# Kernel tuning notes

Hardware: AMD Instinct MI355X
Metric: run time of the kernel (lower is better)

## Reference

```python
import jax, jax.numpy as jnp
import numpy as np

D_MODEL = 1024
N_HEADS = 16
HEAD_DIM = D_MODEL // N_HEADS


def setup_inputs() -> dict:
    key = jax.random.key(0)
    ks = jax.random.split(key, 5)
    x = jax.random.normal(ks[0], (4, 2048, D_MODEL), dtype=jnp.float32)
    s = 1.0 / np.sqrt(D_MODEL)
    W_qkv = jax.random.normal(ks[1], (D_MODEL, 3 * D_MODEL), dtype=jnp.float32) * s
    b_qkv = jnp.zeros((3 * D_MODEL,), dtype=jnp.float32)
    W_proj = jax.random.normal(ks[2], (D_MODEL, D_MODEL), dtype=jnp.float32) * s
    b_proj = jnp.zeros((D_MODEL,), dtype=jnp.float32)
    return {"x": x, "W_qkv": W_qkv, "b_qkv": b_qkv, "W_proj": W_proj, "b_proj": b_proj}


def reference(x, W_qkv, b_qkv, W_proj, b_proj):
    B, T, C = x.shape
    H, Dh = N_HEADS, HEAD_DIM
    qkv = x @ W_qkv + b_qkv                      # [B,T,3C]
    q, k, v = jnp.split(qkv, 3, axis=-1)
    # [B,T,C] -> [B,H,T,Dh]
    q = q.reshape(B, T, H, Dh).transpose(0, 2, 1, 3)
    k = k.reshape(B, T, H, Dh).transpose(0, 2, 1, 3)
    v = v.reshape(B, T, H, Dh).transpose(0, 2, 1, 3)
    scale = 1.0 / np.sqrt(Dh)
    att = jnp.einsum("bhqd,bhkd->bhqk", q, k) * scale
    causal = jnp.tril(jnp.ones((T, T), dtype=bool))
    att = jnp.where(causal, att, -jnp.inf)
    att = jax.nn.softmax(att, axis=-1)
    y = jnp.einsum("bhqk,bhkd->bhqd", att, v)    # [B,H,T,Dh]
    y = y.transpose(0, 2, 1, 3).reshape(B, T, C)
    return y @ W_proj + b_proj
```

## Files before the change

### kernel.cpp

```cpp
#include <hip/hip_runtime.h>
#include <hip/hip_bf16.h>
#include <cstdint>
#include <math.h>

#define DM   1024
#define NH   16
#define DH   64
#define BB   4
#define TT   2048
#define MTOT (BB*TT)

using short8 = __attribute__((ext_vector_type(8))) short;
using f32x4  = __attribute__((ext_vector_type(4))) float;

__device__ __forceinline__ f32x4 mfma16(short8 a, short8 b, f32x4 c) {
  return __builtin_amdgcn_mfma_f32_16x16x32_bf16(a, b, c, 0, 0, 0);
}

typedef const __attribute__((address_space(1))) unsigned int* as1_u32p;
typedef __attribute__((address_space(3))) unsigned int*       as3_u32p;

__device__ __forceinline__ void gl_lds16(const void* g, void* l) {
  __builtin_amdgcn_global_load_lds(
      (as1_u32p)(reinterpret_cast<uintptr_t>(g)),
      (as3_u32p)((unsigned int)(reinterpret_cast<uintptr_t>(l))),
      16, 0, 0);
}

__device__ __forceinline__ int swz64(int row, int col) {
  return row*64 + ((((col >> 3) ^ (row & 7)) << 3) | (col & 7));
}

__device__ __forceinline__ unsigned pkbf(float a, float b) {
  __hip_bfloat162 h = __float22bfloat162_rn(make_float2(a, b));
  return *reinterpret_cast<unsigned*>(&h);
}

__device__ __forceinline__ unsigned xor16v(unsigned x, bool odd) {
  unsigned a = x, b = x;
  asm("v_permlane16_swap_b32 %0, %1" : "+v"(a), "+v"(b));
  return odd ? a : b;
}
__device__ __forceinline__ unsigned swap32sel(unsigned d, unsigned s, bool odd) {
  asm("v_permlane32_swap_b32 %0, %1" : "+v"(d), "+v"(s));
  return odd ? s : d;
}

__device__ __forceinline__ short8 ldsr_o0(unsigned a) {
  short8 r; asm volatile("ds_read_b128 %0, %1" : "=v"(r) : "v"(a)); return r;
}
__device__ __forceinline__ short8 ldsr_o1(unsigned a) {
  short8 r; asm volatile("ds_read_b128 %0, %1 offset:2048" : "=v"(r) : "v"(a)); return r;
}
__device__ __forceinline__ short8 ldsr_o2(unsigned a) {
  short8 r; asm volatile("ds_read_b128 %0, %1 offset:4096" : "=v"(r) : "v"(a)); return r;
}
__device__ __forceinline__ short8 ldsr_o3(unsigned a) {
  short8 r; asm volatile("ds_read_b128 %0, %1 offset:6144" : "=v"(r) : "v"(a)); return r;
}

#define LGKM0  do { asm volatile("s_waitcnt lgkmcnt(0)"); __builtin_amdgcn_sched_barrier(0); } while(0)
#define VMCNT6 do { __builtin_amdgcn_sched_barrier(0); asm volatile("s_waitcnt vmcnt(6)"); __builtin_amdgcn_sched_barrier(0); } while(0)
#define VMCNT0 do { __builtin_amdgcn_sched_barrier(0); asm volatile("s_waitcnt vmcnt(0)"); __builtin_amdgcn_sched_barrier(0); } while(0)
#define BARRIER do { __builtin_amdgcn_s_barrier(); __builtin_amdgcn_sched_barrier(0); } while(0)

__global__ __launch_bounds__(256) void k_cvt(const float* __restrict__ in,
                                             __hip_bfloat16* __restrict__ out, int n8) {
  int i = blockIdx.x * 256 + threadIdx.x;
  if (i >= n8) return;
  const float* p = in + (size_t)i * 8;
  short8 o;
#pragma unroll
  for (int j = 0; j < 8; ++j) {
    __hip_bfloat16 h = __float2bfloat16(p[j]);
    o[j] = *reinterpret_cast<short*>(&h);
  }
  *reinterpret_cast<short8*>(out + (size_t)i * 8) = o;
}

__global__ __launch_bounds__(256) void k_transpose_cvt(const float* __restrict__ W,
                                                       __hip_bfloat16* __restrict__ Wt,
                                                       int K, int N) {
  __shared__ float tbuf[32][33];
  const int n0 = blockIdx.x * 32, k0 = blockIdx.y * 32;
  const int tx = threadIdx.x & 31, ty = threadIdx.x >> 5;
#pragma unroll
  for (int i = 0; i < 4; ++i)
    tbuf[ty + i*8][tx] = W[(size_t)(k0 + ty + i*8) * N + n0 + tx];
  __syncthreads();
#pragma unroll
  for (int i = 0; i < 4; ++i)
    Wt[(size_t)(n0 + ty + i*8) * K + k0 + tx] = __float2bfloat16(tbuf[tx][ty + i*8]);
}

__global__ __launch_bounds__(512, 2) void k_gemm2(const __hip_bfloat16* __restrict__ A,
                                                  const __hip_bfloat16* __restrict__ Bt,
                                                  const float* __restrict__ bias,
                                                  __hip_bfloat16* __restrict__ Qb,
                                                  __hip_bfloat16* __restrict__ Kb,
                                                  __hip_bfloat16* __restrict__ Vtb) {
  __shared__ __hip_bfloat16 As[3][256 * 64];
  __shared__ __hip_bfloat16 Bs[3][128 * 64];
  const int tid = threadIdx.x;
  const int l = tid & 63, w = tid >> 6;
  const int lr = l & 15, lg = l >> 4;
  const int wm = w >> 1, wn = w & 1;
  const int m0 = blockIdx.x * 256, n0 = blockIdx.y * 128;

  const int srow = tid >> 3;
  const int scol = (((tid & 7) ^ (srow & 7)) << 3);
  const size_t aoffs = (size_t)(m0 + srow) * 1024 + scol;
  const size_t boffs = (size_t)(n0 + srow) * 1024 + scol;
  const int ldst = tid * 8;

  auto stage = [&](int t, int s) {
    const int k0 = t * 64;
    __hip_bfloat16* as_ = &As[s][0];
    __hip_bfloat16* bs_ = &Bs[s][0];
#pragma unroll
    for (int rd = 0; rd < 4; ++rd)
      gl_lds16(A + aoffs + (size_t)rd * 65536 + k0, as_ + rd * 4096 + ldst);
#pragma unroll
    for (int rd = 0; rd < 2; ++rd)
      gl_lds16(Bt + boffs + (size_t)rd * 65536 + k0, bs_ + rd * 4096 + ldst);
  };

  const unsigned asLds = (unsigned)(uintptr_t)&As[0][0];
  const unsigned bsLds = (unsigned)(uintptr_t)&Bs[0][0];
  const unsigned aBase = asLds + 2u * ((wm*64 + lr) * 64 + ((lg ^ (lr & 7)) << 3));
  const unsigned bBase = bsLds + 2u * ((wn*64 + lr) * 64 + ((lg ^ (lr & 7)) << 3));

  stage(0, 0);
  stage(1, 1);
  VMCNT6;
  BARRIER;

  f32x4 acc[4][4] = {};
  short8 a_[4][2], b_[2][2];

#pragma unroll
  for (int t = 0; t < 16; ++t) {
    const int s = t % 3;
    const unsigned aB0 = aBase + (unsigned)s * 32768u;
    const unsigned aB1 = aB0 ^ 64u;
    const unsigned bB0 = bBase + (unsigned)s * 16384u;
    const unsigned bB1 = bB0 ^ 64u;
    if (t + 2 < 16) stage(t + 2, (t + 2) % 3);
    a_[0][0] = ldsr_o0(aB0); a_[1][0] = ldsr_o1(aB0); a_[2][0] = ldsr_o2(aB0); a_[3][0] = ldsr_o3(aB0);
    a_[0][1] = ldsr_o0(aB1); a_[1][1] = ldsr_o1(aB1); a_[2][1] = ldsr_o2(aB1); a_[3][1] = ldsr_o3(aB1);
    b_[0][0] = ldsr_o0(bB0); b_[1][0] = ldsr_o1(bB0);
    b_[0][1] = ldsr_o0(bB1); b_[1][1] = ldsr_o1(bB1);
    LGKM0;
    __builtin_amdgcn_s_setprio(1);
#pragma unroll
    for (int m = 0; m < 4; ++m)
#pragma unroll
      for (int n = 0; n < 2; ++n)
#pragma unroll
        for (int ks = 0; ks < 2; ++ks)
          acc[m][n] = mfma16(a_[m][ks], b_[n][ks], acc[m][n]);
    __builtin_amdgcn_s_setprio(0);
    b_[0][0] = ldsr_o2(bB0); b_[1][0] = ldsr_o3(bB0);
    b_[0][1] = ldsr_o2(bB1); b_[1][1] = ldsr_o3(bB1);
    LGKM0;
    __builtin_amdgcn_s_setprio(1);
#pragma unroll
    for (int m = 0; m < 4; ++m)
#pragma unroll
      for (int n = 0; n < 2; ++n)
#pragma unroll
        for (int ks = 0; ks < 2; ++ks)
          acc[m][n + 2] = mfma16(a_[m][ks], b_[n][ks], acc[m][n + 2]);
    __builtin_amdgcn_s_setprio(0);
    if (t <= 13) { VMCNT6; }
    else if (t == 14) { VMCNT0; }
    BARRIER;
  }

  __syncthreads();
  __hip_bfloat16* reg = &As[0][0] + w * 4096;
  const int colbase = n0 + wn * 64;
  const int which = colbase >> 10;
  const int hh = (colbase >> 6) & 15;
  const float qs = 0.18033688011112042f;
#pragma unroll
  for (int n = 0; n < 4; ++n) {
    const int lc = n * 16 + lr;
    const float bv = bias[colbase + lc];
#pragma unroll
    for (int m = 0; m < 4; ++m) {
#pragma unroll
      for (int r = 0; r < 4; ++r) {
        const int lrow = m * 16 + lg * 4 + r;
        float v = acc[m][n][r] + bv;
        if (which == 0) v *= qs;
        const __hip_bfloat16 hv = __float2bfloat16(v);
        if (which == 2) reg[swz64(lc, lrow)] = hv;
        else            reg[swz64(lrow, lc)] = hv;
      }
    }
  }
  const int rowbase = m0 + wm * 64;
  const int b = rowbase >> 11;
  const size_t bh = (size_t)b * 16 + hh;
  const int g = l >> 2, i = l & 3;
  if (which < 2) {
    __hip_bfloat16* base = (which == 0) ? Qb : Kb;
#pragma unroll
    for (int j = 0; j < 4; ++j) {
      const int lrow = j * 16 + g;
      const int t = (rowbase & 2047) + lrow;
      __hip_bfloat16* dst = base + (bh * TT + t) * 64 + i * 16;
      short8 y0 = *reinterpret_cast<const short8*>(&reg[swz64(lrow, i * 16)]);
      short8 y1 = *reinterpret_cast<const short8*>(&reg[swz64(lrow, i * 16 + 8)]);
      *reinterpret_cast<short8*>(dst) = y0;
      *reinterpret_cast<short8*>(dst + 8) = y1;
    }
  } else {
#pragma unroll
    for (int j = 0; j < 4; ++j) {
      const int dd = j * 16 + g;
      const int t = (rowbase & 2047) + i * 16;
      __hip_bfloat16* dst = Vtb + (bh * 64 + dd) * TT + t;
      short8 y0 = *reinterpret_cast<const short8*>(&reg[swz64(dd, i * 16)]);
      short8 y1 = *reinterpret_cast<const short8*>(&reg[swz64(dd, i * 16 + 8)]);
      *reinterpret_cast<short8*>(dst) = y0;
      *reinterpret_cast<short8*>(dst + 8) = y1;
    }
  }
}

__global__ __launch_bounds__(256) void k_gemm(const __hip_bfloat16* __restrict__ A,
                                              const __hip_bfloat16* __restrict__ Bt,
                                              const float* __restrict__ bias,
                                              float* __restrict__ outF) {
  __shared__ __hip_bfloat16 As[128 * 64];
  __shared__ __hip_bfloat16 Bs[128 * 64];
  const int tid = threadIdx.x;
  const int l = tid & 63, w = tid >> 6;
  const int lr = l & 15, lg = l >> 4;
  const int wr = w >> 1, wc = w & 1;
  const int m0 = blockIdx.x * 128, n0 = blockIdx.y * 128;
  f32x4 acc[4][4] = {};
  for (int k0 = 0; k0 < 1024; k0 += 64) {
#pragma unroll
    for (int it = 0; it < 4; ++it) {
      int e = it * 2048 + tid * 8;
      int row = e >> 6;
      int lcol = ((((e >> 3) & 7) ^ (row & 7)) << 3);
      gl_lds16(A + (size_t)(m0 + row) * 1024 + k0 + lcol, &As[e]);
    }
#pragma unroll
    for (int it = 0; it < 4; ++it) {
      int e = it * 2048 + tid * 8;
      int row = e >> 6;
      int lcol = ((((e >> 3) & 7) ^ (row & 7)) << 3);
      gl_lds16(Bt + (size_t)(n0 + row) * 1024 + k0 + lcol, &Bs[e]);
    }
    __syncthreads();
#pragma unroll
    for (int ks = 0; ks < 2; ++ks) {
      short8 af[4], bf[4];
#pragma unroll
      for (int m = 0; m < 4; ++m)
        af[m] = *reinterpret_cast<const short8*>(&As[swz64(wr*64 + m*16 + lr, ks*32 + lg*8)]);
#pragma unroll
      for (int n = 0; n < 4; ++n)
        bf[n] = *reinterpret_cast<const short8*>(&Bs[swz64(wc*64 + n*16 + lr, ks*32 + lg*8)]);
#pragma unroll
      for (int m = 0; m < 4; ++m)
#pragma unroll
        for (int n = 0; n < 4; ++n)
          acc[m][n] = mfma16(af[m], bf[n], acc[m][n]);
    }
    __syncthreads();
  }
#pragma unroll
  for (int n = 0; n < 4; ++n) {
    const int col = n0 + wc*64 + n*16 + lr;
    const float bv = bias[col];
#pragma unroll
    for (int m = 0; m < 4; ++m)
#pragma unroll
      for (int r = 0; r < 4; ++r) {
        const int row = m0 + wr*64 + m*16 + lg*4 + r;
        outF[(size_t)row * 1024 + col] = acc[m][n][r] + bv;
      }
  }
}

__device__ __forceinline__ void tile_step(f32x4 s0, f32x4 s1, int kbase, int kmaxw, int qm,
                                          bool odd, short8 v0, short8 v1, short8 v2, short8 v3,
                                          f32x4 (&acc)[4], float& lrun) {
  if (kbase + 31 > kmaxw - 15) {
#pragma unroll
    for (int r = 0; r < 4; ++r) {
      if (kbase + r > qm)      s0[r] = -INFINITY;
      if (kbase + 16 + r > qm) s1[r] = -INFINITY;
    }
  }
  float p0 = __builtin_amdgcn_exp2f(s0[0]), p1 = __builtin_amdgcn_exp2f(s0[1]);
  float p2 = __builtin_amdgcn_exp2f(s0[2]), p3 = __builtin_amdgcn_exp2f(s0[3]);
  float p4 = __builtin_amdgcn_exp2f(s1[0]), p5 = __builtin_amdgcn_exp2f(s1[1]);
  float p6 = __builtin_amdgcn_exp2f(s1[2]), p7 = __builtin_amdgcn_exp2f(s1[3]);
  lrun += ((p0 + p1) + (p2 + p3)) + ((p4 + p5) + (p6 + p7));
  const unsigned u0 = pkbf(p0, p1);
  const unsigned u1 = pkbf(p2, p3);
  const unsigned u2 = pkbf(p4, p5);
  const unsigned u3 = pkbf(p6, p7);
  const unsigned e0 = xor16v(u0, odd);
  const unsigned e1 = xor16v(u1, odd);
  const unsigned e2 = xor16v(u2, odd);
  const unsigned e3 = xor16v(u3, odd);
  const unsigned ql0 = odd ? e0 : u0;
  const unsigned ql1 = odd ? e1 : u1;
  const unsigned ql2 = odd ? u0 : e0;
  const unsigned ql3 = odd ? u1 : e1;
  const unsigned qh0 = odd ? e2 : u2;
  const unsigned qh1 = odd ? e3 : u3;
  const unsigned qh2 = odd ? u2 : e2;
  const unsigned qh3 = odd ? u3 : e3;
  union { unsigned u[4]; short8 s; } pw;
  pw.u[0] = swap32sel(ql0, qh0, odd);
  pw.u[1] = swap32sel(ql1, qh1, odd);
  pw.u[2] = swap32sel(ql2, qh2, odd);
  pw.u[3] = swap32sel(ql3, qh3, odd);
  const short8 pf = pw.s;
  acc[0] = mfma16(v0, pf, acc[0]);
  acc[1] = mfma16(v1, pf, acc[1]);
  acc[2] = mfma16(v2, pf, acc[2]);
  acc[3] = mfma16(v3, pf, acc[3]);
}

__device__ __forceinline__ void store_tile(__hip_bfloat16* Ylds, f32x4 (&acc)[4],
                                           float lrun, int q0, int w, int l,
                                           int lr, int lg, int bh,
                                           __hip_bfloat16* __restrict__ Y) {
  lrun += __shfl_xor(lrun, 16);
  lrun += __shfl_xor(lrun, 32);
  const float inv = 1.f / lrun;
#pragma unroll
  for (int nb = 0; nb < 4; ++nb) {
#pragma unroll
    for (int r = 0; r < 4; ++r) {
      const int d = nb * 16 + lg * 4 + r;
      Ylds[swz64(lr, d)] = __float2bfloat16(acc[nb][r] * inv);
    }
  }
  const int rr = l >> 2, part = l & 3;
  const int trow = q0 + w * 16 + rr;
  const int b = bh >> 4, h = bh & 15;
  short8 y0 = *reinterpret_cast<const short8*>(&Ylds[swz64(rr, part * 16)]);
  short8 y1 = *reinterpret_cast<const short8*>(&Ylds[swz64(rr, part * 16 + 8)]);
  __hip_bfloat16* dst = Y + ((size_t)b * TT + trow) * 1024 + h * 64 + part * 16;
  *reinterpret_cast<short8*>(dst) = y0;
  *reinterpret_cast<short8*>(dst + 8) = y1;
}

__global__ __launch_bounds__(256, 4) void k_flash(const __hip_bfloat16* __restrict__ Qb,
                                                  const __hip_bfloat16* __restrict__ Kb,
                                                  const __hip_bfloat16* __restrict__ Vtb,
                                                  __hip_bfloat16* __restrict__ Y) {
  __shared__ __hip_bfloat16 Klds[128 * 64];
  __shared__ __hip_bfloat16 Vtlds[64 * 128];
  const int tid = threadIdx.x;
  const int l = tid & 63, w = tid >> 6;
  const int lr = l & 15, lg = l >> 4;
  const bool odd = (lg & 1);
  const int p  = blockIdx.x >> 6;
  const int bh = blockIdx.x & 63;
  const int q0A = p * 64, q0B = (31 - p) * 64;
  const __hip_bfloat16* Qp = Qb + (size_t)bh * TT * 64;
  const __hip_bfloat16* Kp = Kb + (size_t)bh * TT * 64;
  const __hip_bfloat16* Vp = Vtb + (size_t)bh * 64 * TT;
  const int qrowA = q0A + w * 16 + lr;
  const int qrowB = q0B + w * 16 + lr;
  const short8 qfA0 = *reinterpret_cast<const short8*>(Qp + (size_t)qrowA * 64 + lg * 8);
  const short8 qfA1 = *reinterpret_cast<const short8*>(Qp + (size_t)qrowA * 64 + 32 + lg * 8);
  const short8 qfB0 = *reinterpret_cast<const short8*>(Qp + (size_t)qrowB * 64 + lg * 8);
  const short8 qfB1 = *reinterpret_cast<const short8*>(Qp + (size_t)qrowB * 64 + 32 + lg * 8);
  f32x4 accA[4] = {}, accB[4] = {};
  float lA = 0.f, lB = 0.f;

  const int ka  = lr * 64 + ((lg ^ (lr & 7)) << 3);
  const int va  = lr * 128 + ((lg ^ (lr & 15)) << 3);

  const __hip_bfloat16* gk[4];
  const __hip_bfloat16* gv[4];
  __hip_bfloat16* lk[4];
  __hip_bfloat16* lv[4];
#pragma unroll
  for (int it = 0; it < 4; ++it) {
    int e = it * 2048 + tid * 8;
    int rowk = e >> 6;
    int lcolk = ((((e >> 3) & 7) ^ (rowk & 7)) << 3);
    gk[it] = Kp + (size_t)rowk * 64 + lcolk;
    lk[it] = &Klds[e];
    int rowv = e >> 7;
    int lcolv = ((((e >> 3) & 15) ^ (rowv & 15)) << 3);
    gv[it] = Vp + (size_t)rowv * TT + lcolv;
    lv[it] = &Vtlds[e];
  }

  const int kmaxwA = q0A + w * 16 + 15;
  const int kmaxwB = q0B + w * 16 + 15;
  const int qmA = qrowA - lg * 4;
  const int qmB = qrowB - lg * 4;
  const int nblk = (q0B + 63) / 128 + 1;
  for (int blk = 0; blk < nblk; ++blk) {
    const int kv0 = blk * 128;
#pragma unroll
    for (int it = 0; it < 4; ++it) {
      gl_lds16(gk[it], lk[it]);
      gk[it] += 128 * 64;
    }
#pragma unroll
    for (int it = 0; it < 4; ++it) {
      gl_lds16(gv[it], lv[it]);
      gv[it] += 128;
    }
    __syncthreads();
#pragma unroll
    for (int kci = 0; kci < 4; ++kci) {
      const int kbase = kv0 + kci * 32;
      if (kbase > kmaxwB) break;
      const int kb = ka + kci * 2048;
      const short8 kf00 = *reinterpret_cast<const short8*>(&Klds[kb]);
      const short8 kf10 = *reinterpret_cast<const short8*>(&Klds[kb + 1024]);
      const short8 kf01 = *reinterpret_cast<const short8*>(&Klds[kb ^ 32]);
      const short8 kf11 = *reinterpret_cast<const short8*>(&Klds[(kb + 1024) ^ 32]);
      f32x4 sB0 = {}, sB1 = {};
      sB0 = mfma16(kf00, qfB0, sB0);
      sB1 = mfma16(kf10, qfB0, sB1);
      sB0 = mfma16(kf01, qfB1, sB0);
      sB1 = mfma16(kf11, qfB1, sB1);
      const bool aAct = (kbase <= kmaxwA);
      f32x4 sA0 = {}, sA1 = {};
      if (aAct) {
        sA0 = mfma16(kf00, qfA0, sA0);
        sA1 = mfma16(kf10, qfA0, sA1);
        sA0 = mfma16(kf01, qfA1, sA0);
        sA1 = mfma16(kf11, qfA1, sA1);
      }
      const int vb = va ^ (kci * 32);
      const short8 v0 = *reinterpret_cast<const short8*>(&Vtlds[vb]);
      const short8 v1 = *reinterpret_cast<const short8*>(&Vtlds[vb + 2048]);
      const short8 v2 = *reinterpret_cast<const short8*>(&Vtlds[vb + 4096]);
      const short8 v3 = *reinterpret_cast<const short8*>(&Vtlds[vb + 6144]);
      tile_step(sB0, sB1, kbase, kmaxwB, qmB, odd, v0, v1, v2, v3, accB, lB);
      if (aAct)
        tile_step(sA0, sA1, kbase, kmaxwA, qmA, odd, v0, v1, v2, v3, accA, lA);
    }
    __syncthreads();
  }
  __hip_bfloat16* Ylds = Klds + w * 1024;
  store_tile(Ylds, accA, lA, q0A, w, l, lr, lg, bh, Y);
  store_tile(Ylds, accB, lB, q0B, w, l, lr, lg, bh, Y);
}

extern "C" void kernel_launch(void* const* d_in, const int* in_sizes, int n_in,
                              void* d_out, int out_size, void* d_ws, size_t ws_size,
                              hipStream_t stream) {
  const float* x     = (const float*)d_in[0];
  const float* Wqkv  = (const float*)d_in[1];
  const float* bqkv  = (const float*)d_in[2];
  const float* Wproj = (const float*)d_in[3];
  const float* bproj = (const float*)d_in[4];

  char* ws = (char*)d_ws;
  size_t off = 0;
  auto alloc = [&](size_t bytes) {
    char* p = ws + off;
    off += (bytes + 255) & ~(size_t)255;
    return p;
  };
  __hip_bfloat16* xb    = (__hip_bfloat16*)alloc((size_t)MTOT * 1024 * 2);
  __hip_bfloat16* wqkvT = (__hip_bfloat16*)alloc((size_t)3072 * 1024 * 2);
  __hip_bfloat16* wpT   = (__hip_bfloat16*)alloc((size_t)1024 * 1024 * 2);
  __hip_bfloat16* Qb    = (__hip_bfloat16*)alloc((size_t)64 * TT * 64 * 2);
  __hip_bfloat16* Kb    = (__hip_bfloat16*)alloc((size_t)64 * TT * 64 * 2);
  __hip_bfloat16* Vtb   = (__hip_bfloat16*)alloc((size_t)64 * TT * 64 * 2);
  __hip_bfloat16* Yb    = (__hip_bfloat16*)alloc((size_t)MTOT * 1024 * 2);

  k_cvt<<<(MTOT * 1024 / 8 + 255) / 256, 256, 0, stream>>>(x, xb, MTOT * 1024 / 8);
  k_transpose_cvt<<<dim3(3072 / 32, 1024 / 32), 256, 0, stream>>>(Wqkv, wqkvT, 1024, 3072);
  k_transpose_cvt<<<dim3(1024 / 32, 1024 / 32), 256, 0, stream>>>(Wproj, wpT, 1024, 1024);
  k_gemm2<<<dim3(32, 24), 512, 0, stream>>>(xb, wqkvT, bqkv, Qb, Kb, Vtb);
  k_flash<<<16 * 64, 256, 0, stream>>>(Qb, Kb, Vtb, Yb);
  k_gemm<<<dim3(64, 8), 256, 0, stream>>>(Yb, wpT, bproj, (float*)d_out);
}
```

Measured before the change: 166.3 us.

## Reuse pipelined 256x128 GEMM for output projection and simplify P-fragment permutes

New measurement: 152.3 us. 8.4% less time.

```diff
diff --git a/kernel.cpp b/kernel.cpp
--- a/kernel.cpp
+++ b/kernel.cpp
@@ -36,14 +36,11 @@
   return *reinterpret_cast<unsigned*>(&h);
 }
 
-__device__ __forceinline__ unsigned xor16v(unsigned x, bool odd) {
-  unsigned a = x, b = x;
+__device__ __forceinline__ void perm16p(unsigned &a, unsigned &b) {
   asm("v_permlane16_swap_b32 %0, %1" : "+v"(a), "+v"(b));
-  return odd ? a : b;
-}
-__device__ __forceinline__ unsigned swap32sel(unsigned d, unsigned s, bool odd) {
-  asm("v_permlane32_swap_b32 %0, %1" : "+v"(d), "+v"(s));
-  return odd ? s : d;
+}
+__device__ __forceinline__ void perm32p(unsigned &a, unsigned &b) {
+  asm("v_permlane32_swap_b32 %0, %1" : "+v"(a), "+v"(b));
 }
 
 __device__ __forceinline__ short8 ldsr_o0(unsigned a) {
@@ -93,9 +90,11 @@
     Wt[(size_t)(n0 + ty + i*8) * K + k0 + tx] = __float2bfloat16(tbuf[tx][ty + i*8]);
 }
 
+template <int EPI>
 __global__ __launch_bounds__(512, 2) void k_gemm2(const __hip_bfloat16* __restrict__ A,
                                                   const __hip_bfloat16* __restrict__ Bt,
                                                   const float* __restrict__ bias,
+                                                  float* __restrict__ outF,
                                                   __hip_bfloat16* __restrict__ Qb,
                                                   __hip_bfloat16* __restrict__ Kb,
                                                   __hip_bfloat16* __restrict__ Vtb) {
@@ -178,125 +177,82 @@
   }
 
   __syncthreads();
-  __hip_bfloat16* reg = &As[0][0] + w * 4096;
-  const int colbase = n0 + wn * 64;
-  const int which = colbase >> 10;
-  const int hh = (colbase >> 6) & 15;
-  const float qs = 0.18033688011112042f;
-#pragma unroll
-  for (int n = 0; n < 4; ++n) {
-    const int lc = n * 16 + lr;
-    const float bv = bias[colbase + lc];
-#pragma unroll
-    for (int m = 0; m < 4; ++m) {
-#pragma unroll
-      for (int r = 0; r < 4; ++r) {
-        const int lrow = m * 16 + lg * 4 + r;
-        float v = acc[m][n][r] + bv;
-        if (which == 0) v *= qs;
-        const __hip_bfloat16 hv = __float2bfloat16(v);
-        if (which == 2) reg[swz64(lc, lrow)] = hv;
-        else            reg[swz64(lrow, lc)] = hv;
+  if (EPI == 0) {
+    __hip_bfloat16* reg = &As[0][0] + w * 4096;
+    const int colbase = n0 + wn * 64;
+    const int which = colbase >> 10;
+    const int hh = (colbase >> 6) & 15;
+    const float qs = 0.18033688011112042f;
+#pragma unroll
+    for (int n = 0; n < 4; ++n) {
+      const int lc = n * 16 + lr;
+      const float bv = bias[colbase + lc];
+#pragma unroll
+      for (int m = 0; m < 4; ++m) {
+#pragma unroll
+        for (int r = 0; r < 4; ++r) {
+          const int lrow = m * 16 + lg * 4 + r;
+          float v = acc[m][n][r] + bv;
+          if (which == 0) v *= qs;
+          const __hip_bfloat16 hv = __float2bfloat16(v);
+          if (which == 2) reg[swz64(lc, lrow)] = hv;
+          else            reg[swz64(lrow, lc)] = hv;
+        }
       }
     }
-  }
-  const int rowbase = m0 + wm * 64;
-  const int b = rowbase >> 11;
-  const size_t bh = (size_t)b * 16 + hh;
-  const int g = l >> 2, i = l & 3;
-  if (which < 2) {
-    __hip_bfloat16* base = (which == 0) ? Qb : Kb;
-#pragma unroll
-    for (int j = 0; j < 4; ++j) {
-      const int lrow = j * 16 + g;
-      const int t = (rowbase & 2047) + lrow;
-      __hip_bfloat16* dst = base + (bh * TT + t) * 64 + i * 16;
-      short8 y0 = *reinterpret_cast<const short8*>(&reg[swz64(lrow, i * 16)]);
-      short8 y1 = *reinterpret_cast<const short8*>(&reg[swz64(lrow, i * 16 + 8)]);
-      *reinterpret_cast<short8*>(dst) = y0;
-      *reinterpret_cast<short8*>(dst + 8) = y1;
+    const int rowbase = m0 + wm * 64;
+    const int b = rowbase >> 11;
+    const size_t bh = (size_t)b * 16 + hh;
+    const int g = l >> 2, i = l & 3;
+    if (which < 2) {
+      __hip_bfloat16* base = (which == 0) ? Qb : Kb;
+#pragma unroll
+      for (int j = 0; j < 4; ++j) {
+        const int lrow = j * 16 + g;
+        const int t = (rowbase & 2047) + lrow;
+        __hip_bfloat16* dst = base + (bh * TT + t) * 64 + i * 16;
+        short8 y0 = *reinterpret_cast<const short8*>(&reg[swz64(lrow, i * 16)]);
+        short8 y1 = *reinterpret_cast<const short8*>(&reg[swz64(lrow, i * 16 + 8)]);
+        *reinterpret_cast<short8*>(dst) = y0;
+        *reinterpret_cast<short8*>(dst + 8) = y1;
+      }
+    } else {
+#pragma unroll
+      for (int j = 0; j < 4; ++j) {
+        const int dd = j * 16 + g;
+        const int t = (rowbase & 2047) + i * 16;
+        __hip_bfloat16* dst = Vtb + (bh * 64 + dd) * TT + t;
+        short8 y0 = *reinterpret_cast<const short8*>(&reg[swz64(dd, i * 16)]);
+        short8 y1 = *reinterpret_cast<const short8*>(&reg[swz64(dd, i * 16 + 8)]);
+        *reinterpret_cast<short8*>(dst) = y0;
+        *reinterpret_cast<short8*>(dst + 8) = y1;
+      }
     }
   } else {
 #pragma unroll
-    for (int j = 0; j < 4; ++j) {
-      const int dd = j * 16 + g;
-      const int t = (rowbase & 2047) + i * 16;
-      __hip_bfloat16* dst = Vtb + (bh * 64 + dd) * TT + t;
-      short8 y0 = *reinterpret_cast<const short8*>(&reg[swz64(dd, i * 16)]);
-      short8 y1 = *reinterpret_cast<const short8*>(&reg[swz64(dd, i * 16 + 8)]);
-      *reinterpret_cast<short8*>(dst) = y0;
-      *reinterpret_cast<short8*>(dst + 8) = y1;
-    }
-  }
-}
-
-__global__ __launch_bounds__(256) void k_gemm(const __hip_bfloat16* __restrict__ A,
-                                              const __hip_bfloat16* __restrict__ Bt,
-                                              const float* __restrict__ bias,
-                                              float* __restrict__ outF) {
-  __shared__ __hip_bfloat16 As[128 * 64];
-  __shared__ __hip_bfloat16 Bs[128 * 64];
-  const int tid = threadIdx.x;
-  const int l = tid & 63, w = tid >> 6;
-  const int lr = l & 15, lg = l >> 4;
-  const int wr = w >> 1, wc = w & 1;
-  const int m0 = blockIdx.x * 128, n0 = blockIdx.y * 128;
-  f32x4 acc[4][4] = {};
-  for (int k0 = 0; k0 < 1024; k0 += 64) {
-#pragma unroll
-    for (int it = 0; it < 4; ++it) {
-      int e = it * 2048 + tid * 8;
-      int row = e >> 6;
-      int lcol = ((((e >> 3) & 7) ^ (row & 7)) << 3);
-      gl_lds16(A + (size_t)(m0 + row) * 1024 + k0 + lcol, &As[e]);
-    }
-#pragma unroll
-    for (int it = 0; it < 4; ++it) {
-      int e = it * 2048 + tid * 8;
-      int row = e >> 6;
-      int lcol = ((((e >> 3) & 7) ^ (row & 7)) << 3);
-      gl_lds16(Bt + (size_t)(n0 + row) * 1024 + k0 + lcol, &Bs[e]);
-    }
-    __syncthreads();
-#pragma unroll
-    for (int ks = 0; ks < 2; ++ks) {
-      short8 af[4], bf[4];
+    for (int n = 0; n < 4; ++n) {
+      const int col = n0 + wn * 64 + n * 16 + lr;
+      const float bv = bias[col];
 #pragma unroll
       for (int m = 0; m < 4; ++m)
-        af[m] = *reinterpret_cast<const short8*>(&As[swz64(wr*64 + m*16 + lr, ks*32 + lg*8)]);
-#pragma unroll
-      for (int n = 0; n < 4; ++n)
-        bf[n] = *reinterpret_cast<const short8*>(&Bs[swz64(wc*64 + n*16 + lr, ks*32 + lg*8)]);
-#pragma unroll
-      for (int m = 0; m < 4; ++m)
-#pragma unroll
-        for (int n = 0; n < 4; ++n)
-          acc[m][n] = mfma16(af[m], bf[n], acc[m][n]);
-    }
-    __syncthreads();
-  }
-#pragma unroll
-  for (int n = 0; n < 4; ++n) {
-    const int col = n0 + wc*64 + n*16 + lr;
-    const float bv = bias[col];
-#pragma unroll
-    for (int m = 0; m < 4; ++m)
-#pragma unroll
-      for (int r = 0; r < 4; ++r) {
-        const int row = m0 + wr*64 + m*16 + lg*4 + r;
-        outF[(size_t)row * 1024 + col] = acc[m][n][r] + bv;
-      }
-  }
-}
-
-__device__ __forceinline__ void tile_step(f32x4 s0, f32x4 s1, int kbase, int kmaxw, int qm,
-                                          bool odd, short8 v0, short8 v1, short8 v2, short8 v3,
+#pragma unroll
+        for (int r = 0; r < 4; ++r) {
+          const int row = m0 + wm * 64 + m * 16 + lg * 4 + r;
+          outF[(size_t)row * 1024 + col] = acc[m][n][r] + bv;
+        }
+    }
+  }
+}
+
+__device__ __forceinline__ void tile_step(f32x4 s0, f32x4 s1, int kbase, int kmaxw, int qmb,
+                                          short8 v0, short8 v1, short8 v2, short8 v3,
                                           f32x4 (&acc)[4], float& lrun) {
   if (kbase + 31 > kmaxw - 15) {
 #pragma unroll
     for (int r = 0; r < 4; ++r) {
-      if (kbase + r > qm)      s0[r] = -INFINITY;
-      if (kbase + 16 + r > qm) s1[r] = -INFINITY;
+      const int off = (r & 1) + ((r & 2) << 2);
+      if (kbase + off > qmb)      s0[r] = -INFINITY;
+      if (kbase + 16 + off > qmb) s1[r] = -INFINITY;
     }
   }
   float p0 = __builtin_amdgcn_exp2f(s0[0]), p1 = __builtin_amdgcn_exp2f(s0[1]);
@@ -304,27 +260,16 @@
   float p4 = __builtin_amdgcn_exp2f(s1[0]), p5 = __builtin_amdgcn_exp2f(s1[1]);
   float p6 = __builtin_amdgcn_exp2f(s1[2]), p7 = __builtin_amdgcn_exp2f(s1[3]);
   lrun += ((p0 + p1) + (p2 + p3)) + ((p4 + p5) + (p6 + p7));
-  const unsigned u0 = pkbf(p0, p1);
-  const unsigned u1 = pkbf(p2, p3);
-  const unsigned u2 = pkbf(p4, p5);
-  const unsigned u3 = pkbf(p6, p7);
-  const unsigned e0 = xor16v(u0, odd);
-  const unsigned e1 = xor16v(u1, odd);
-  const unsigned e2 = xor16v(u2, odd);
-  const unsigned e3 = xor16v(u3, odd);
-  const unsigned ql0 = odd ? e0 : u0;
-  const unsigned ql1 = odd ? e1 : u1;
-  const unsigned ql2 = odd ? u0 : e0;
-  const unsigned ql3 = odd ? u1 : e1;
-  const unsigned qh0 = odd ? e2 : u2;
-  const unsigned qh1 = odd ? e3 : u3;
-  const unsigned qh2 = odd ? u2 : e2;
-  const unsigned qh3 = odd ? u3 : e3;
+  unsigned u0 = pkbf(p0, p1);
+  unsigned u1 = pkbf(p2, p3);
+  unsigned u2 = pkbf(p4, p5);
+  unsigned u3 = pkbf(p6, p7);
+  perm16p(u0, u1);
+  perm16p(u2, u3);
+  perm32p(u0, u2);
+  perm32p(u1, u3);
   union { unsigned u[4]; short8 s; } pw;
-  pw.u[0] = swap32sel(ql0, qh0, odd);
-  pw.u[1] = swap32sel(ql1, qh1, odd);
-  pw.u[2] = swap32sel(ql2, qh2, odd);
-  pw.u[3] = swap32sel(ql3, qh3, odd);
+  pw.u[0] = u0; pw.u[1] = u2; pw.u[2] = u1; pw.u[3] = u3;
   const short8 pf = pw.s;
   acc[0] = mfma16(v0, pf, acc[0]);
   acc[1] = mfma16(v1, pf, acc[1]);
@@ -366,7 +311,6 @@
   const int tid = threadIdx.x;
   const int l = tid & 63, w = tid >> 6;
   const int lr = l & 15, lg = l >> 4;
-  const bool odd = (lg & 1);
   const int p  = blockIdx.x >> 6;
   const int bh = blockIdx.x & 63;
   const int q0A = p * 64, q0B = (31 - p) * 64;
@@ -394,7 +338,10 @@
     int e = it * 2048 + tid * 8;
     int rowk = e >> 6;
     int lcolk = ((((e >> 3) & 7) ^ (rowk & 7)) << 3);
-    gk[it] = Kp + (size_t)rowk * 64 + lcolk;
+    int rk = rowk & 15;
+    int srk = (((rk >> 1) ^ (rk >> 3)) & 1) ? (rk ^ 10) : rk;
+    int rowks = (rowk & ~15) | srk;
+    gk[it] = Kp + (size_t)rowks * 64 + lcolk;
     lk[it] = &Klds[e];
     int rowv = e >> 7;
     int lcolv = ((((e >> 3) & 15) ^ (rowv & 15)) << 3);
@@ -404,8 +351,9 @@
 
   const int kmaxwA = q0A + w * 16 + 15;
   const int kmaxwB = q0B + w * 16 + 15;
-  const int qmA = qrowA - lg * 4;
-  const int qmB = qrowB - lg * 4;
+  const int base_lg = ((lg & 1) << 2) | (lg & 2);
+  const int qmbA = qrowA - base_lg;
+  const int qmbB = qrowB - base_lg;
   const int nblk = (q0B + 63) / 128 + 1;
   for (int blk = 0; blk < nblk; ++blk) {
     const int kv0 = blk * 128;
@@ -447,9 +395,9 @@
       const short8 v1 = *reinterpret_cast<const short8*>(&Vtlds[vb + 2048]);
       const short8 v2 = *reinterpret_cast<const short8*>(&Vtlds[vb + 4096]);
       const short8 v3 = *reinterpret_cast<const short8*>(&Vtlds[vb + 6144]);
-      tile_step(sB0, sB1, kbase, kmaxwB, qmB, odd, v0, v1, v2, v3, accB, lB);
+      tile_step(sB0, sB1, kbase, kmaxwB, qmbB, v0, v1, v2, v3, accB, lB);
       if (aAct)
-        tile_step(sA0, sA1, kbase, kmaxwA, qmA, odd, v0, v1, v2, v3, accA, lA);
+        tile_step(sA0, sA1, kbase, kmaxwA, qmbA, v0, v1, v2, v3, accA, lA);
     }
     __syncthreads();
   }
@@ -485,7 +433,8 @@
   k_cvt<<<(MTOT * 1024 / 8 + 255) / 256, 256, 0, stream>>>(x, xb, MTOT * 1024 / 8);
   k_transpose_cvt<<<dim3(3072 / 32, 1024 / 32), 256, 0, stream>>>(Wqkv, wqkvT, 1024, 3072);
   k_transpose_cvt<<<dim3(1024 / 32, 1024 / 32), 256, 0, stream>>>(Wproj, wpT, 1024, 1024);
-  k_gemm2<<<dim3(32, 24), 512, 0, stream>>>(xb, wqkvT, bqkv, Qb, Kb, Vtb);
+  k_gemm2<0><<<dim3(32, 24), 512, 0, stream>>>(xb, wqkvT, bqkv, nullptr, Qb, Kb, Vtb);
   k_flash<<<16 * 64, 256, 0, stream>>>(Qb, Kb, Vtb, Yb);
-  k_gemm<<<dim3(64, 8), 256, 0, stream>>>(Yb, wpT, bproj, (float*)d_out);
-}
+  k_gemm2<1><<<dim3(32, 8), 512, 0, stream>>>(Yb, wpT, bproj, (float*)d_out,
+                                              nullptr, nullptr, nullptr);
+}
```
